# Optimization experiments

Hardware: AMD Instinct MI355X
Metric: run time of the kernel (lower is better)

The kernel has to match this reference:

```python
import jax, jax.numpy as jnp
import numpy as np

B, DIM, IMG, HEADS, DH = 8, 512, 32, 8, 64
INNER = HEADS * DH  # == DIM, required by final reshape(b, n, c)
N = IMG * IMG
BN_EPS = 1e-5


def setup_inputs() -> dict:
    key = jax.random.key(0)
    ks = jax.random.split(key, 11)
    s = lambda k, sh: jax.random.normal(k, sh, jnp.float32) * 0.05
    return {
        "x": jax.random.normal(ks[0], (B, N, DIM), jnp.float32),
        # stacked q/k/v params, index 0=q, 1=k, 2=v
        "dw_w": s(ks[1], (3, DIM, 1, 3, 3)),   # depthwise conv kernels (OIHW, groups=DIM)
        "dw_b": s(ks[2], (3, DIM)),
        "bn_g": jnp.ones((3, DIM), jnp.float32) + s(ks[3], (3, DIM)),
        "bn_b": s(ks[4], (3, DIM)),
        "bn_m": s(ks[5], (3, DIM)),
        "bn_v": jnp.abs(jax.random.normal(ks[6], (3, DIM), jnp.float32)) + 1.0,
        "pw_w": s(ks[7], (3, INNER, DIM)),     # pointwise 1x1 conv weights
        "pw_b": s(ks[8], (3, INNER)),
        "out_w": s(ks[9], (DIM, INNER)),       # nn.Linear weight [out, in]
        "out_b": s(ks[10], (DIM,)),
    }


def _proj(x_img, dw_w, dw_b, bn_g, bn_b, bn_m, bn_v, pw_w, pw_b):
    # depthwise 3x3 conv, stride 1, pad 1
    y = jax.lax.conv_general_dilated(
        x_img, dw_w, (1, 1), [(1, 1), (1, 1)],
        dimension_numbers=("NCHW", "OIHW", "NCHW"), feature_group_count=DIM)
    y = y + dw_b[None, :, None, None]
    # eval-mode BatchNorm2d
    scale = bn_g / jnp.sqrt(bn_v + BN_EPS)
    y = (y - bn_m[None, :, None, None]) * scale[None, :, None, None] + bn_b[None, :, None, None]
    # pointwise 1x1 conv
    y = jnp.einsum("bchw,oc->bohw", y, pw_w) + pw_b[None, :, None, None]
    return y


def reference(x, dw_w, dw_b, bn_g, bn_b, bn_m, bn_v, pw_w, pw_b, out_w, out_b):
    b = x.shape[0]
    # b (l w) c -> b c l w
    xi = x.transpose(0, 2, 1).reshape(b, DIM, IMG, IMG)
    # q, k, v: b (h d) l w -> b h (l w) d
    qkv = [
        _proj(xi, dw_w[i], dw_b[i], bn_g[i], bn_b[i], bn_m[i], bn_v[i], pw_w[i], pw_b[i])
        .reshape(b, HEADS, DH, N).transpose(0, 1, 3, 2)
        for i in range(3)
    ]
    q, k, v = qkv
    att = jax.nn.softmax(jnp.einsum("bhnd,bhmd->bhnm", q, k) * (DH ** -0.5), axis=-1)
    out = jnp.einsum("bhnm,bhmd->bhnd", att, v)  # [b,h,n,d]
    out = out.transpose(0, 2, 1, 3).reshape(b, N, INNER)
    return out @ out_w.T + out_b  # to_out Linear (dropout=0)
```

## Files before the change

### kernel.cpp

```cpp
#include <hip/hip_runtime.h>
#include <hip/hip_bf16.h>

#define BB    8
#define DIMC  512
#define IMGS  32
#define NPIX  1024
#define NHEAD 8
#define DHEAD 64

typedef __attribute__((ext_vector_type(8))) short short8;
typedef __attribute__((ext_vector_type(4))) float float4v;
typedef __attribute__((ext_vector_type(2))) _Float16 half2v;
typedef __attribute__((ext_vector_type(4))) _Float16 half4v;

__device__ __forceinline__ float b2f(unsigned short u) {
  union { unsigned int i; float f; } c;
  c.i = ((unsigned int)u) << 16;
  return c.f;
}
__device__ __forceinline__ unsigned short f2b(float f) {
  union { float f; unsigned int u; } c;
  c.f = f;
  unsigned int r = c.u + 0x7fffu + ((c.u >> 16) & 1u);
  return (unsigned short)(r >> 16);
}
__device__ __forceinline__ unsigned short f2h(float f) {
  union { _Float16 h; unsigned short u; } c;
  c.h = (_Float16)f;
  return c.u;
}

__device__ __forceinline__ void storeC(float* p, float v) { *p = v; }
__device__ __forceinline__ void storeC(unsigned short* p, float v) { *p = f2b(v); }

__device__ __forceinline__ void async16(const void* g, void* l) {
  __builtin_amdgcn_global_load_lds(
      (const __attribute__((address_space(1))) void*)g,
      (__attribute__((address_space(3))) void*)l, 16, 0, 0);
}

__global__ __launch_bounds__(256) void wcvt_kernel(
    const float* __restrict__ pw_w, const float* __restrict__ out_w,
    const float* __restrict__ pw_b, const float* __restrict__ dw_w,
    const float* __restrict__ dw_b, const float* __restrict__ bn_g,
    const float* __restrict__ bn_b, const float* __restrict__ bn_m,
    const float* __restrict__ bn_v, unsigned short* __restrict__ wbf,
    float* __restrict__ bb, float* __restrict__ wT,
    float* __restrict__ shiftv) {
  const int i4 = (blockIdx.x * 256 + threadIdx.x) * 4;
  float4 v = (i4 < 3 * DIMC * DIMC)
                 ? *reinterpret_cast<const float4*>(pw_w + i4)
                 : *reinterpret_cast<const float4*>(out_w + (i4 - 3 * DIMC * DIMC));
  const float sc = (i4 < DIMC * DIMC) ? 0.125f : 1.0f;
  ushort4 o;
  o.x = f2b(v.x * sc); o.y = f2b(v.y * sc); o.z = f2b(v.z * sc); o.w = f2b(v.w * sc);
  *reinterpret_cast<ushort4*>(wbf + i4) = o;
  const int idx = blockIdx.x * 256 + threadIdx.x;
  if (idx < 6 * 256) {
    if (idx < 3 * DIMC / 2) {
      #pragma unroll
      for (int hh = 0; hh < 2; ++hh) {
        const int id2 = idx * 2 + hh;
        const int i = id2 >> 9, c = id2 & 511;
        const float scale = bn_g[id2] * rsqrtf(bn_v[id2] + 1e-5f);
        shiftv[id2] = (dw_b[id2] - bn_m[id2]) * scale + bn_b[id2];
        #pragma unroll
        for (int t = 0; t < 9; ++t)
          wT[(i * 9 + t) * DIMC + c] = dw_w[(size_t)id2 * 9 + t] * scale;
      }
    }
    if (idx < 3 * DIMC)
      bb[idx] = pw_b[idx] * (idx < DIMC ? 0.125f : 1.0f);
  }
}

__global__ __launch_bounds__(256) void dwbn_kernel(
    const float* __restrict__ x, const float* __restrict__ wT,
    const float* __restrict__ shiftv, unsigned short* __restrict__ z) {
  const int wp = blockIdx.x, lg = blockIdx.y, b = blockIdx.z;
  const int t = threadIdx.x;
  const int c = (t & 127) * 4;
  const int w = wp * 2 + (t >> 7);
  const int l0 = lg * 4;
  const float* xb = x + (size_t)b * NPIX * DIMC + c;

  const float4 zero4 = make_float4(0.f, 0.f, 0.f, 0.f);
  float4 win[6][3];
  #pragma unroll
  for (int rr = 0; rr < 6; ++rr) {
    const int l = l0 - 1 + rr;
    #pragma unroll
    for (int dw = 0; dw < 3; ++dw) {
      const int ww = w - 1 + dw;
      const bool ok = ((unsigned)l < IMGS) && ((unsigned)ww < IMGS);
      win[rr][dw] = ok ? *reinterpret_cast<const float4*>(
                             xb + (size_t)(l * IMGS + ww) * DIMC)
                       : zero4;
    }
  }

  #pragma unroll
  for (int i = 0; i < 3; ++i) {
    float4 wv[9];
    #pragma unroll
    for (int tp = 0; tp < 9; ++tp)
      wv[tp] = *reinterpret_cast<const float4*>(wT + (i * 9 + tp) * DIMC + c);
    const float4 sh = *reinterpret_cast<const float4*>(shiftv + i * DIMC + c);
    #pragma unroll
    for (int r = 0; r < 4; ++r) {
      float a0 = sh.x, a1 = sh.y, a2 = sh.z, a3 = sh.w;
      #pragma unroll
      for (int kh = 0; kh < 3; ++kh)
        #pragma unroll
        for (int kw = 0; kw < 3; ++kw) {
          const float4 wq = wv[kh * 3 + kw];
          const float4 xq = win[r + kh][kw];
          a0 = fmaf(wq.x, xq.x, a0);
          a1 = fmaf(wq.y, xq.y, a1);
          a2 = fmaf(wq.z, xq.z, a2);
          a3 = fmaf(wq.w, xq.w, a3);
        }
      ushort4 st;
      st.x = f2b(a0); st.y = f2b(a1); st.z = f2b(a2); st.w = f2b(a3);
      *reinterpret_cast<ushort4*>(
          z + (((size_t)(i * BB + b)) * NPIX + (l0 + r) * IMGS + w) * DIMC + c) = st;
    }
  }
}

template <typename CT>
__global__ __launch_bounds__(256) void gemm_mfma(
    const unsigned short* __restrict__ Abase,
    const unsigned short* __restrict__ Wbase,
    const float* __restrict__ biasBase, CT* __restrict__ Cbase) {
  __shared__ short As[8 * 64 * 8];
  __shared__ short Bs[8 * 64 * 8];
  const int bz = blockIdx.z;
  const int wi = bz >> 3;
  const short* A = (const short*)Abase + (size_t)bz * NPIX * DIMC;
  const short* W = (const short*)Wbase + (size_t)wi * DIMC * DIMC;
  const float* bias = biasBase + wi * DIMC;
  CT* C = Cbase + (size_t)bz * NPIX * DIMC;

  const int t = threadIdx.x;
  const int wv = t >> 6, lane = t & 63;
  const int lo = lane & 15, hi = lane >> 4;
  const int wm = wv >> 1, wn = wv & 1;
  const int m0 = blockIdx.y * 128, n0 = blockIdx.x * 128;

  float4v acc[4][4];
  #pragma unroll
  for (int i = 0; i < 4; ++i)
    #pragma unroll
    for (int j = 0; j < 4; ++j) acc[i][j] = {0.f, 0.f, 0.f, 0.f};

  for (int k0 = 0; k0 < DIMC; k0 += 32) {
    #pragma unroll
    for (int p = 0; p < 2; ++p) {
      const int sub = wv + p * 4;
      async16(A + (size_t)(m0 + sub * 16 + lo) * DIMC + k0 + hi * 8,
              As + (sub * 64 + lane) * 8);
      async16(W + (size_t)(n0 + sub * 16 + lo) * DIMC + k0 + hi * 8,
              Bs + (sub * 64 + lane) * 8);
    }
    __syncthreads();
    short8 af[4], bf[4];
    #pragma unroll
    for (int mt = 0; mt < 4; ++mt)
      af[mt] = *reinterpret_cast<const short8*>(As + ((wm * 4 + mt) * 64 + lane) * 8);
    #pragma unroll
    for (int nt = 0; nt < 4; ++nt)
      bf[nt] = *reinterpret_cast<const short8*>(Bs + ((wn * 4 + nt) * 64 + lane) * 8);
    #pragma unroll
    for (int mt = 0; mt < 4; ++mt)
      #pragma unroll
      for (int nt = 0; nt < 4; ++nt)
        acc[mt][nt] = __builtin_amdgcn_mfma_f32_16x16x32_bf16(af[mt], bf[nt],
                                                              acc[mt][nt], 0, 0, 0);
    __syncthreads();
  }

  float bv[4];
  #pragma unroll
  for (int nt = 0; nt < 4; ++nt) bv[nt] = bias[n0 + wn * 64 + nt * 16 + lo];
  #pragma unroll
  for (int mt = 0; mt < 4; ++mt) {
    #pragma unroll
    for (int r = 0; r < 4; ++r) {
      const int row = m0 + wm * 64 + mt * 16 + hi * 4 + r;
      CT* cp = C + (size_t)row * DIMC + n0 + wn * 64 + lo;
      #pragma unroll
      for (int nt = 0; nt < 4; ++nt) storeC(cp + nt * 16, acc[mt][nt][r] + bv[nt]);
    }
  }
}

__global__ __launch_bounds__(256) void vt_kernel(
    const unsigned short* __restrict__ v, unsigned short* __restrict__ vt) {
  __shared__ unsigned short tile[64][68];
  const int n0 = blockIdx.x * 64, h = blockIdx.y, b = blockIdx.z;
  const int t = threadIdx.x;
  const unsigned short* vb = v + (size_t)b * NPIX * DIMC + h * DHEAD;
  #pragma unroll
  for (int u = 0; u < 4; ++u) {
    const int lin = t + u * 256;
    const int row = lin >> 4, c4 = (lin & 15) * 4;
    *reinterpret_cast<ushort4*>(&tile[row][c4]) =
        *reinterpret_cast<const ushort4*>(vb + (size_t)(n0 + row) * DIMC + c4);
  }
  __syncthreads();
  unsigned short* vtb = vt + ((size_t)(b * NHEAD + h)) * DHEAD * NPIX;
  #pragma unroll
  for (int u = 0; u < 4; ++u) {
    const int lin = t + u * 256;
    const int d = lin >> 4, n4 = (lin & 15) * 4;
    ushort4 o;
    o.x = f2h(b2f(tile[n4 + 0][d]));
    o.y = f2h(b2f(tile[n4 + 1][d]));
    o.z = f2h(b2f(tile[n4 + 2][d]));
    o.w = f2h(b2f(tile[n4 + 3][d]));
    *reinterpret_cast<ushort4*>(vtb + (size_t)d * NPIX + n0 + n4) = o;
  }
}

__global__ __launch_bounds__(256, 3) void attn_mfma(
    const unsigned short* __restrict__ qkv, const unsigned short* __restrict__ vt,
    unsigned short* __restrict__ attn_o) {
  __shared__ char sm[17664];
  const int b = blockIdx.x, h = blockIdx.y, qt = blockIdx.z;
  const int t = threadIdx.x;
  const int wv = t >> 6, lane = t & 63;
  const int lo = lane & 15, hi = lane >> 4;

  const short* qb = (const short*)qkv + ((size_t)(0 * BB + b) * NPIX) * DIMC + h * DHEAD;
  const short* kb = (const short*)qkv + ((size_t)(1 * BB + b) * NPIX) * DIMC + h * DHEAD;
  const _Float16* vth =
      (const _Float16*)vt + ((size_t)(b * NHEAD + h)) * DHEAD * NPIX;

  short8 qf[4][2];
  #pragma unroll
  for (int mt = 0; mt < 4; ++mt)
    #pragma unroll
    for (int cc = 0; cc < 2; ++cc)
      qf[mt][cc] = *reinterpret_cast<const short8*>(
          qb + (size_t)(qt * 64 + mt * 16 + lo) * DIMC + cc * 32 + hi * 8);

  float4v oacc[4][4];
  float lsumv[4] = {0.f, 0.f, 0.f, 0.f};
  #pragma unroll
  for (int mt = 0; mt < 4; ++mt)
    #pragma unroll
    for (int dt = 0; dt < 4; ++dt) oacc[mt][dt] = {0.f, 0.f, 0.f, 0.f};

  const int kw0 = wv * 256;
  for (int it = 0; it < 16; ++it) {
    const int k0 = kw0 + it * 16;
    const short8 kf0 =
        *reinterpret_cast<const short8*>(kb + (size_t)(k0 + lo) * DIMC + hi * 8);
    const short8 kf1 =
        *reinterpret_cast<const short8*>(kb + (size_t)(k0 + lo) * DIMC + 32 + hi * 8);
    half4v vf[4];
    #pragma unroll
    for (int dt = 0; dt < 4; ++dt)
      vf[dt] = *reinterpret_cast<const half4v*>(
          vth + (size_t)(dt * 16 + lo) * NPIX + k0 + hi * 4);

    float4v sacc[4];
    #pragma unroll
    for (int mt = 0; mt < 4; ++mt) {
      sacc[mt] = {0.f, 0.f, 0.f, 0.f};
      sacc[mt] = __builtin_amdgcn_mfma_f32_16x16x32_bf16(kf0, qf[mt][0], sacc[mt], 0, 0, 0);
      sacc[mt] = __builtin_amdgcn_mfma_f32_16x16x32_bf16(kf1, qf[mt][1], sacc[mt], 0, 0, 0);
    }

    half4v pf[4];
    #pragma unroll
    for (int mt = 0; mt < 4; ++mt) {
      const float p0 = __expf(sacc[mt][0]);
      const float p1 = __expf(sacc[mt][1]);
      const float p2 = __expf(sacc[mt][2]);
      const float p3 = __expf(sacc[mt][3]);
      lsumv[mt] += (p0 + p1) + (p2 + p3);
      const half2v a01 =
          __builtin_bit_cast(half2v, __builtin_amdgcn_cvt_pkrtz(p0, p1));
      const half2v a23 =
          __builtin_bit_cast(half2v, __builtin_amdgcn_cvt_pkrtz(p2, p3));
      pf[mt] = half4v{a01[0], a01[1], a23[0], a23[1]};
    }

    #pragma unroll
    for (int mt = 0; mt < 4; ++mt)
      #pragma unroll
      for (int dt = 0; dt < 4; ++dt)
        oacc[mt][dt] = __builtin_amdgcn_mfma_f32_16x16x16f16(pf[mt], vf[dt],
                                                             oacc[mt][dt], 0, 0, 0);
  }

  #pragma unroll
  for (int mt = 0; mt < 4; ++mt) {
    float v = lsumv[mt];
    v += __shfl_xor(v, 16);
    v += __shfl_xor(v, 32);
    lsumv[mt] = v;
  }

  float* Obuf = (float*)sm;
  float* lbuf = (float*)(sm + 16384);
  float* linv = (float*)(sm + 17408);
  if (hi == 0) {
    #pragma unroll
    for (int mt = 0; mt < 4; ++mt) lbuf[wv * 64 + mt * 16 + lo] = lsumv[mt];
  }
  __syncthreads();
  if (t < 64) linv[t] = 1.0f / (lbuf[t] + lbuf[64 + t] + lbuf[128 + t] + lbuf[192 + t]);

  unsigned short* aob = attn_o + ((size_t)b * NPIX + qt * 64) * DIMC + h * DHEAD;
  #pragma unroll
  for (int mt = 0; mt < 4; ++mt) {
    __syncthreads();
    #pragma unroll
    for (int dt = 0; dt < 4; ++dt)
      #pragma unroll
      for (int r = 0; r < 4; ++r)
        Obuf[wv * 1024 + (dt * 4 + r) * 64 + lane] = oacc[mt][dt][r];
    __syncthreads();
    #pragma unroll
    for (int k2 = 0; k2 < 4; ++k2) {
      const int e = t + k2 * 256;
      const float sum2 = Obuf[e] + Obuf[1024 + e] + Obuf[2048 + e] + Obuf[3072 + e];
      const int dt = e >> 8, r = (e >> 6) & 3, le = e & 63;
      const int row = mt * 16 + (le >> 4) * 4 + r, d = dt * 16 + (le & 15);
      aob[(size_t)row * DIMC + d] = f2b(sum2 * linv[row]);
    }
  }
}

extern "C" void kernel_launch(void* const* d_in, const int* in_sizes, int n_in,
                              void* d_out, int out_size, void* d_ws, size_t ws_size,
                              hipStream_t stream) {
  const float* x    = (const float*)d_in[0];
  const float* dw_w = (const float*)d_in[1];
  const float* dw_b = (const float*)d_in[2];
  const float* bn_g = (const float*)d_in[3];
  const float* bn_b = (const float*)d_in[4];
  const float* bn_m = (const float*)d_in[5];
  const float* bn_v = (const float*)d_in[6];
  const float* pw_w = (const float*)d_in[7];
  const float* pw_b = (const float*)d_in[8];
  const float* out_w = (const float*)d_in[9];
  const float* out_b = (const float*)d_in[10];
  float* out = (float*)d_out;

  unsigned short* z   = (unsigned short*)d_ws;
  unsigned short* qkv = z + (size_t)3 * BB * NPIX * DIMC;
  unsigned short* wbf = qkv + (size_t)3 * BB * NPIX * DIMC;
  float* bb = (float*)(wbf + (size_t)4 * DIMC * DIMC);
  float* wT = bb + 3 * DIMC;
  float* shiftv = wT + 3 * 9 * DIMC;
  unsigned short* vtb = z;
  unsigned short* attn_o = z + (size_t)BB * NHEAD * DHEAD * NPIX;

  wcvt_kernel<<<dim3(1024), 256, 0, stream>>>(pw_w, out_w, pw_b, dw_w, dw_b,
                                              bn_g, bn_b, bn_m, bn_v, wbf, bb,
                                              wT, shiftv);
  dwbn_kernel<<<dim3(16, 8, BB), 256, 0, stream>>>(x, wT, shiftv, z);
  gemm_mfma<unsigned short><<<dim3(4, 8, 24), 256, 0, stream>>>(z, wbf, bb, qkv);
  vt_kernel<<<dim3(16, NHEAD, BB), 256, 0, stream>>>(
      qkv + (size_t)2 * BB * NPIX * DIMC, vtb);
  attn_mfma<<<dim3(BB, NHEAD, 16), 256, 0, stream>>>(qkv, vtb, attn_o);
  gemm_mfma<float><<<dim3(4, 8, 8), 256, 0, stream>>>(
      attn_o, wbf + (size_t)3 * DIMC * DIMC, out_b, out);
}
```

Baseline: 215.5 us.

## Prefetch K/V fragments one step ahead and fold log2e into Q scale

The attention loop now double-buffers K and V register fragments, loading the next 16-key step while the current step's MFMAs and exponentials run, and the loop is fully unrolled. The softmax scale constant absorbs log2(e) into the Q projection weights and bias, so the kernel can use the native exp2 instruction instead of __expf. Launch bounds rise from 3 to 4 blocks per SM. This aims to hide global-load latency and cut the exp cost, at the price of more registers under a tighter occupancy cap, which could cause spills.

```diff
diff --git a/kernel.cpp b/kernel.cpp
--- a/kernel.cpp
+++ b/kernel.cpp
@@ -7,6 +7,8 @@
 #define NPIX  1024
 #define NHEAD 8
 #define DHEAD 64
+
+#define QSCALE 0.18033688011112042f
 
 typedef __attribute__((ext_vector_type(8))) short short8;
 typedef __attribute__((ext_vector_type(4))) float float4v;
@@ -51,7 +53,7 @@
   float4 v = (i4 < 3 * DIMC * DIMC)
                  ? *reinterpret_cast<const float4*>(pw_w + i4)
                  : *reinterpret_cast<const float4*>(out_w + (i4 - 3 * DIMC * DIMC));
-  const float sc = (i4 < DIMC * DIMC) ? 0.125f : 1.0f;
+  const float sc = (i4 < DIMC * DIMC) ? QSCALE : 1.0f;
   ushort4 o;
   o.x = f2b(v.x * sc); o.y = f2b(v.y * sc); o.z = f2b(v.z * sc); o.w = f2b(v.w * sc);
   *reinterpret_cast<ushort4*>(wbf + i4) = o;
@@ -70,7 +72,7 @@
       }
     }
     if (idx < 3 * DIMC)
-      bb[idx] = pw_b[idx] * (idx < DIMC ? 0.125f : 1.0f);
+      bb[idx] = pw_b[idx] * (idx < DIMC ? QSCALE : 1.0f);
   }
 }
 
@@ -223,7 +225,7 @@
   }
 }
 
-__global__ __launch_bounds__(256, 3) void attn_mfma(
+__global__ __launch_bounds__(256, 4) void attn_mfma(
     const unsigned short* __restrict__ qkv, const unsigned short* __restrict__ vt,
     unsigned short* __restrict__ attn_o) {
   __shared__ char sm[17664];
@@ -253,33 +255,43 @@
     for (int dt = 0; dt < 4; ++dt) oacc[mt][dt] = {0.f, 0.f, 0.f, 0.f};
 
   const int kw0 = wv * 256;
+
+  short8 kfb[2][2];
+  half4v vfb[2][4];
+  auto load_stage = [&](int st, int k0) {
+    kfb[st][0] =
+        *reinterpret_cast<const short8*>(kb + (size_t)(k0 + lo) * DIMC + hi * 8);
+    kfb[st][1] =
+        *reinterpret_cast<const short8*>(kb + (size_t)(k0 + lo) * DIMC + 32 + hi * 8);
+    #pragma unroll
+    for (int dt = 0; dt < 4; ++dt)
+      vfb[st][dt] = *reinterpret_cast<const half4v*>(
+          vth + (size_t)(dt * 16 + lo) * NPIX + k0 + hi * 4);
+  };
+
+  load_stage(0, kw0);
+  #pragma unroll
   for (int it = 0; it < 16; ++it) {
-    const int k0 = kw0 + it * 16;
-    const short8 kf0 =
-        *reinterpret_cast<const short8*>(kb + (size_t)(k0 + lo) * DIMC + hi * 8);
-    const short8 kf1 =
-        *reinterpret_cast<const short8*>(kb + (size_t)(k0 + lo) * DIMC + 32 + hi * 8);
-    half4v vf[4];
-    #pragma unroll
-    for (int dt = 0; dt < 4; ++dt)
-      vf[dt] = *reinterpret_cast<const half4v*>(
-          vth + (size_t)(dt * 16 + lo) * NPIX + k0 + hi * 4);
+    const int cur = it & 1, nxt = cur ^ 1;
+    if (it < 15) load_stage(nxt, kw0 + (it + 1) * 16);
 
     float4v sacc[4];
     #pragma unroll
     for (int mt = 0; mt < 4; ++mt) {
       sacc[mt] = {0.f, 0.f, 0.f, 0.f};
-      sacc[mt] = __builtin_amdgcn_mfma_f32_16x16x32_bf16(kf0, qf[mt][0], sacc[mt], 0, 0, 0);
-      sacc[mt] = __builtin_amdgcn_mfma_f32_16x16x32_bf16(kf1, qf[mt][1], sacc[mt], 0, 0, 0);
+      sacc[mt] = __builtin_amdgcn_mfma_f32_16x16x32_bf16(kfb[cur][0], qf[mt][0],
+                                                         sacc[mt], 0, 0, 0);
+      sacc[mt] = __builtin_amdgcn_mfma_f32_16x16x32_bf16(kfb[cur][1], qf[mt][1],
+                                                         sacc[mt], 0, 0, 0);
     }
 
     half4v pf[4];
     #pragma unroll
     for (int mt = 0; mt < 4; ++mt) {
-      const float p0 = __expf(sacc[mt][0]);
-      const float p1 = __expf(sacc[mt][1]);
-      const float p2 = __expf(sacc[mt][2]);
-      const float p3 = __expf(sacc[mt][3]);
+      const float p0 = __builtin_amdgcn_exp2f(sacc[mt][0]);
+      const float p1 = __builtin_amdgcn_exp2f(sacc[mt][1]);
+      const float p2 = __builtin_amdgcn_exp2f(sacc[mt][2]);
+      const float p3 = __builtin_amdgcn_exp2f(sacc[mt][3]);
       lsumv[mt] += (p0 + p1) + (p2 + p3);
       const half2v a01 =
           __builtin_bit_cast(half2v, __builtin_amdgcn_cvt_pkrtz(p0, p1));
@@ -292,7 +304,7 @@
     for (int mt = 0; mt < 4; ++mt)
       #pragma unroll
       for (int dt = 0; dt < 4; ++dt)
-        oacc[mt][dt] = __builtin_amdgcn_mfma_f32_16x16x16f16(pf[mt], vf[dt],
+        oacc[mt][dt] = __builtin_amdgcn_mfma_f32_16x16x16f16(pf[mt], vfb[cur][dt],
                                                              oacc[mt][dt], 0, 0, 0);
   }
 
```

New measurement: 404.9 us. 1.88x slower.
